# Performance work log

Measured on AMD Instinct MI355X. Metric: run time of the kernel, lower is better.

Reference implementation:

```python
import jax, jax.numpy as jnp
import numpy as np

EMBED = 1024
HEADS = 16
HEAD_DIM = EMBED // HEADS


def setup_inputs() -> dict:
    key = jax.random.key(0)
    ks = jax.random.split(key, 9)
    s = 1.0 / np.sqrt(EMBED)
    inp = {
        "inputs": jax.random.normal(ks[0], (2, 2048, EMBED), dtype=jnp.float32),
        "Wq": jax.random.normal(ks[1], (EMBED, EMBED), dtype=jnp.float32) * s,
        "bq": jnp.zeros((EMBED,), dtype=jnp.float32),
        "Wk": jax.random.normal(ks[2], (EMBED, EMBED), dtype=jnp.float32) * s,
        "bk": jnp.zeros((EMBED,), dtype=jnp.float32),
        "Wv": jax.random.normal(ks[3], (EMBED, EMBED), dtype=jnp.float32) * s,
        "bv": jnp.zeros((EMBED,), dtype=jnp.float32),
        "Wo": jax.random.normal(ks[4], (EMBED, EMBED), dtype=jnp.float32) * s,
        "bo": jnp.zeros((EMBED,), dtype=jnp.float32),
    }
    return inp


def _split_heads(x, B, S):
    # [B, S, E] -> [B, H, S, D]
    return x.reshape(B, S, HEADS, HEAD_DIM).transpose(0, 2, 1, 3)


def reference(inputs, Wq, bq, Wk, bk, Wv, bv, Wo, bo):
    B, S, E = inputs.shape
    q = _split_heads(inputs @ Wq + bq, B, S)
    k = _split_heads(inputs @ Wk + bk, B, S)
    v = _split_heads(inputs @ Wv + bv, B, S)
    # scaled dot-product attention per the original: score scaled by sqrt(d_k)
    score = jnp.einsum("bhsd,bhtd->bhst", q, k) / jnp.sqrt(jnp.float32(HEAD_DIM))
    weights = jax.nn.softmax(score, axis=-1)
    attn = jnp.einsum("bhst,bhtd->bhsd", weights, v)
    concat = attn.transpose(0, 2, 1, 3).reshape(B, S, E)
    return concat @ Wo + bo
```

## Files before the change

### kernel.cpp

```cpp
#include <hip/hip_runtime.h>
#include <cmath>

#define EMBED 1024
#define HEADS 16
#define HDIM  64
#define BATCH 2
#define SEQ   2048
#define MTOT  (BATCH*SEQ)
#define KDIM  1024

typedef __attribute__((ext_vector_type(8))) short bf16x8;
typedef __attribute__((ext_vector_type(4))) float fx4;

#define MFMA(a,b,c) __builtin_amdgcn_mfma_f32_16x16x32_bf16((a),(b),(c),0,0,0)

__device__ __forceinline__ unsigned short f2bf(float x) {
    unsigned u = __float_as_uint(x);
    unsigned r = (u + 0x7FFFu + ((u >> 16) & 1u)) >> 16;
    return (unsigned short)r;
}
__device__ __forceinline__ float bf2f(unsigned short h) {
    return __uint_as_float(((unsigned)h) << 16);
}
__device__ __forceinline__ int swz_grp(int row, int grp) {
    return row * 64 + ((grp ^ (row & 7)) << 3);
}
__device__ __forceinline__ void gload16(const void* g, void* l) {
    __builtin_amdgcn_global_load_lds((const __attribute__((address_space(1))) void*)g,
                                     (__attribute__((address_space(3))) void*)l, 16, 0, 0);
}
__device__ __forceinline__ float dpp_qswap(float x) {
    return __int_as_float(__builtin_amdgcn_mov_dpp(__float_as_int(x), 0xB1, 0xF, 0xF, true));
}

#define C2S 0.18033688f

__global__ __launch_bounds__(256)
void prep(const float* __restrict__ X,
          const float* __restrict__ Wq, const float* __restrict__ Wk,
          const float* __restrict__ Wv, const float* __restrict__ Wo,
          unsigned short* __restrict__ Xh,
          unsigned short* __restrict__ WtH, unsigned short* __restrict__ WtOh)
{
    const int bid = blockIdx.x;
    const int tid = threadIdx.x;
    if (bid < 2048) {
        int i = (bid * 256 + tid) * 8;
        float4 a = *(const float4*)(X + i);
        float4 b = *(const float4*)(X + i + 4);
        bf16x8 h;
        h[0] = (short)f2bf(a.x); h[1] = (short)f2bf(a.y);
        h[2] = (short)f2bf(a.z); h[3] = (short)f2bf(a.w);
        h[4] = (short)f2bf(b.x); h[5] = (short)f2bf(b.y);
        h[6] = (short)f2bf(b.z); h[7] = (short)f2bf(b.w);
        *(bf16x8*)(Xh + i) = h;
        return;
    }
    const int u = bid - 2048;
    const int z = u >> 8;
    const float* W = (z == 0) ? Wq : (z == 1) ? Wk : (z == 2) ? Wv : Wo;
    unsigned short* Th = (z < 3) ? WtH + (size_t)z * 1048576 : WtOh;
    const int k0 = ((u >> 4) & 15) * 64, n0 = (u & 15) * 64;

    __shared__ float t[64][65];
    #pragma unroll
    for (int it = 0; it < 4; ++it) {
        int v2 = tid + it * 256;
        int r = v2 >> 4, c4 = (v2 & 15) << 2;
        float4 v = *(const float4*)(W + (size_t)(k0 + r) * EMBED + n0 + c4);
        t[r][c4] = v.x; t[r][c4 + 1] = v.y; t[r][c4 + 2] = v.z; t[r][c4 + 3] = v.w;
    }
    __syncthreads();
    #pragma unroll
    for (int it = 0; it < 4; ++it) {
        int v2 = tid + it * 256;
        int r = v2 >> 4, c4 = (v2 & 15) << 2;
        ushort4 h;
        h.x = f2bf(t[c4 + 0][r]);
        h.y = f2bf(t[c4 + 1][r]);
        h.z = f2bf(t[c4 + 2][r]);
        h.w = f2bf(t[c4 + 3][r]);
        *(ushort4*)(Th + (size_t)(n0 + r) * EMBED + k0 + c4) = h;
    }
}

__global__ __launch_bounds__(256, 4)
void gemm_qkv(const unsigned short* __restrict__ Xh,
              const unsigned short* __restrict__ WtH,
              const float* __restrict__ bq, const float* __restrict__ bk,
              const float* __restrict__ bv,
              unsigned short* __restrict__ Qh, unsigned short* __restrict__ Khi,
              unsigned short* __restrict__ Vhi)
{
    __shared__ unsigned short Ah[8192];
    __shared__ unsigned short Bh[4096];

    const int tid = threadIdx.x, lane = tid & 63, w = tid >> 6;
    const int wm = w >> 1, wn = w & 1;
    const int which = blockIdx.y;
    const int lin = (blockIdx.x & 7) * 64 + (blockIdx.x >> 3);
    const int m0 = (lin >> 4) * 128, n0 = (lin & 15) * 64;

    const char* aB  = (const char*)(Xh + (size_t)m0 * KDIM);
    const char* bB  = (const char*)(WtH + (size_t)which * 1048576 + (size_t)n0 * KDIM);

    auto stageA = [&](int kt) {
        #pragma unroll
        for (int i = 0; i < 4; ++i) {
            int uw = (i << 12) + (w << 10);
            int u  = uw + (lane << 4);
            int row = u >> 7, grp = (u >> 4) & 7;
            size_t gb = (size_t)row * (KDIM * 2) + (size_t)kt * 128 + ((grp ^ (row & 7)) << 4);
            gload16(aB + gb, (char*)Ah + uw);
        }
    };
    auto stageB = [&](int kt) {
        #pragma unroll
        for (int i = 0; i < 2; ++i) {
            int uw = (i << 12) + (w << 10);
            int u  = uw + (lane << 4);
            int row = u >> 7, grp = (u >> 4) & 7;
            size_t gb = (size_t)row * (KDIM * 2) + (size_t)kt * 128 + ((grp ^ (row & 7)) << 4);
            gload16(bB + gb, (char*)Bh + uw);
        }
    };

    const fx4 zero4 = {0.f, 0.f, 0.f, 0.f};
    fx4 acc[4][2];
    #pragma unroll
    for (int i = 0; i < 4; ++i) { acc[i][0] = zero4; acc[i][1] = zero4; }

    for (int kt = 0; kt < KDIM / 64; ++kt) {
        __syncthreads();
        stageA(kt);
        stageB(kt);
        __syncthreads();
        #pragma unroll
        for (int kh = 0; kh < 2; ++kh) {
            const int grp = kh * 4 + (lane >> 4);
            bf16x8 ah[4], bh2[2];
            #pragma unroll
            for (int mi = 0; mi < 4; ++mi)
                ah[mi] = *(const bf16x8*)(Ah + swz_grp(wm * 64 + mi * 16 + (lane & 15), grp));
            #pragma unroll
            for (int ni = 0; ni < 2; ++ni)
                bh2[ni] = *(const bf16x8*)(Bh + swz_grp(wn * 32 + ni * 16 + (lane & 15), grp));
            #pragma unroll
            for (int mi = 0; mi < 4; ++mi)
                #pragma unroll
                for (int ni = 0; ni < 2; ++ni)
                    acc[mi][ni] = MFMA(ah[mi], bh2[ni], acc[mi][ni]);
        }
    }

    const int hh = n0 >> 6;
    const float* bias = (which == 0) ? bq : (which == 1) ? bk : bv;
    #pragma unroll
    for (int mi = 0; mi < 4; ++mi)
        #pragma unroll
        for (int ni = 0; ni < 2; ++ni) {
            const int n = n0 + wn * 32 + ni * 16 + (lane & 15);
            const float bb = bias[n];
            const int d = n & 63;
            if (which < 2) {
                unsigned short* plane = (which == 0) ? Qh : Khi;
                #pragma unroll
                for (int reg = 0; reg < 4; ++reg) {
                    const int m = m0 + wm * 64 + mi * 16 + (lane >> 4) * 4 + reg;
                    const int b = m >> 11, s = m & (SEQ - 1);
                    float val = acc[mi][ni][reg] + bb;
                    if (which == 0) val *= C2S;
                    plane[((size_t)(b * HEADS + hh) * SEQ + s) * HDIM + d] = f2bf(val);
                }
            } else {
                const int m = m0 + wm * 64 + mi * 16 + (lane >> 4) * 4;
                const int b = m >> 11, s = m & (SEQ - 1);
                const int sl = s & 63;
                const int c = (sl & 32) | ((sl & 12) << 1) | ((sl & 16) >> 2);
                ushort4 o;
                o.x = f2bf(acc[mi][ni][0] + bb);
                o.y = f2bf(acc[mi][ni][1] + bb);
                o.z = f2bf(acc[mi][ni][2] + bb);
                o.w = f2bf(acc[mi][ni][3] + bb);
                *(ushort4*)(Vhi + ((size_t)(b * HEADS + hh) * HDIM + d) * SEQ
                            + (s & ~63) + c) = o;
            }
        }
}

__global__ __launch_bounds__(256, 4)
void gemm_ao(const unsigned short* __restrict__ AOh,
             const unsigned short* __restrict__ Bgh,
             const float* __restrict__ bias, float* __restrict__ Cf)
{
    __shared__ unsigned short Ah[8192];
    __shared__ unsigned short Bh[4096];

    const int tid = threadIdx.x, lane = tid & 63, w = tid >> 6;
    const int wm = w >> 1, wn = w & 1;
    const int lin = (blockIdx.x & 7) * 64 + (blockIdx.x >> 3);
    const int m0 = (lin >> 4) * 128, n0 = (lin & 15) * 64;

    const char* aB = (const char*)(AOh + (size_t)m0 * KDIM);
    const char* bB = (const char*)(Bgh + (size_t)n0 * KDIM);

    auto stageA = [&](int kt) {
        #pragma unroll
        for (int i = 0; i < 4; ++i) {
            int uw = (i << 12) + (w << 10);
            int u  = uw + (lane << 4);
            int row = u >> 7, grp = (u >> 4) & 7;
            size_t gb = (size_t)row * (KDIM * 2) + (size_t)kt * 128 + ((grp ^ (row & 7)) << 4);
            gload16(aB + gb, (char*)Ah + uw);
        }
    };
    auto stageB = [&](int kt) {
        #pragma unroll
        for (int i = 0; i < 2; ++i) {
            int uw = (i << 12) + (w << 10);
            int u  = uw + (lane << 4);
            int row = u >> 7, grp = (u >> 4) & 7;
            size_t gb = (size_t)row * (KDIM * 2) + (size_t)kt * 128 + ((grp ^ (row & 7)) << 4);
            gload16(bB + gb, (char*)Bh + uw);
        }
    };

    const fx4 zero4 = {0.f, 0.f, 0.f, 0.f};
    fx4 acc[4][2];
    #pragma unroll
    for (int i = 0; i < 4; ++i) { acc[i][0] = zero4; acc[i][1] = zero4; }

    for (int kt = 0; kt < KDIM / 64; ++kt) {
        __syncthreads();
        stageA(kt);
        stageB(kt);
        __syncthreads();
        #pragma unroll
        for (int kh = 0; kh < 2; ++kh) {
            const int grp = kh * 4 + (lane >> 4);
            bf16x8 ah[4], bh2[2];
            #pragma unroll
            for (int mi = 0; mi < 4; ++mi)
                ah[mi] = *(const bf16x8*)(Ah + swz_grp(wm * 64 + mi * 16 + (lane & 15), grp));
            #pragma unroll
            for (int ni = 0; ni < 2; ++ni)
                bh2[ni] = *(const bf16x8*)(Bh + swz_grp(wn * 32 + ni * 16 + (lane & 15), grp));
            #pragma unroll
            for (int mi = 0; mi < 4; ++mi)
                #pragma unroll
                for (int ni = 0; ni < 2; ++ni)
                    acc[mi][ni] = MFMA(ah[mi], bh2[ni], acc[mi][ni]);
        }
    }

    #pragma unroll
    for (int mi = 0; mi < 4; ++mi)
        #pragma unroll
        for (int ni = 0; ni < 2; ++ni) {
            const int n = n0 + wn * 32 + ni * 16 + (lane & 15);
            const float bb = bias[n];
            #pragma unroll
            for (int reg = 0; reg < 4; ++reg) {
                const int m = m0 + wm * 64 + mi * 16 + (lane >> 4) * 4 + reg;
                Cf[(size_t)m * EMBED + n] = acc[mi][ni][reg] + bb;
            }
        }
}

__global__ __launch_bounds__(256, 4)
void attn_mfma(const unsigned short* __restrict__ Qh,
               const unsigned short* __restrict__ Khi,
               const unsigned short* __restrict__ Vhi, unsigned short* __restrict__ AOh)
{
    __shared__ unsigned short Ks[2][4096];
    __shared__ unsigned short Vs[2][4096];

    const int tid = threadIdx.x, lane = tid & 63, w = tid >> 6;
    const int xcd = blockIdx.x & 7, loc = blockIdx.x >> 3;
    const int bh = xcd * 4 + (loc >> 5);
    const int q0 = (loc & 31) * 64;
    const size_t qkBase = (size_t)bh * SEQ * HDIM;

    auto stageKV = [&](int kv0, int buf) {
        const char* baseK = (const char*)(Khi + qkBase + (size_t)kv0 * HDIM);
        const char* baseV = (const char*)(Vhi + (size_t)bh * HDIM * SEQ + kv0);
        #pragma unroll
        for (int i = 0; i < 2; ++i) {
            int uw = (i << 12) + (w << 10);
            int u  = uw + (lane << 4);
            int row = u >> 7, grp = (u >> 4) & 7;
            size_t gk = (size_t)row * 128 + ((grp ^ (row & 7)) << 4);
            size_t gv = (size_t)row * (SEQ * 2) + ((grp ^ (row & 7)) << 4);
            gload16(baseK + gk, (char*)Ks[buf] + uw);
            gload16(baseV + gv, (char*)Vs[buf] + uw);
        }
    };

    bf16x8 qf[2];
    #pragma unroll
    for (int kh = 0; kh < 2; ++kh) {
        const int row = q0 + w * 16 + (lane & 15);
        const int grp = kh * 4 + (lane >> 4);
        qf[kh] = *(const bf16x8*)(Qh + qkBase + (size_t)row * HDIM + grp * 8);
    }

    const fx4 zero4 = {0.f, 0.f, 0.f, 0.f};
    fx4 acco[4];
    fx4 accl = zero4;
    #pragma unroll
    for (int df = 0; df < 4; ++df) acco[df] = zero4;

    bf16x8 ones;
    #pragma unroll
    for (int i = 0; i < 8; ++i) ones[i] = (short)0x3F80;

    stageKV(0, 0);
    __syncthreads();

    for (int t = 0; t < 32; ++t) {
        const int cur = t & 1;
        if (t < 31) stageKV((t + 1) * 64, cur ^ 1);

        fx4 s4[4] = {zero4, zero4, zero4, zero4};
        __builtin_amdgcn_s_setprio(1);
        #pragma unroll
        for (int kh = 0; kh < 2; ++kh) {
            const int grp = kh * 4 + (lane >> 4);
            bf16x8 kf[4];
            #pragma unroll
            for (int nf = 0; nf < 4; ++nf)
                kf[nf] = *(const bf16x8*)(Ks[cur] + swz_grp(nf * 16 + (lane & 15), grp));
            #pragma unroll
            for (int nf = 0; nf < 4; ++nf)
                s4[nf] = MFMA(kf[nf], qf[kh], s4[nf]);
        }
        __builtin_amdgcn_s_setprio(0);

        float p[4][4];
        #pragma unroll
        for (int kvf = 0; kvf < 4; ++kvf)
            #pragma unroll
            for (int reg = 0; reg < 4; ++reg) {
                float e;
                asm("v_exp_f32 %0, %1\n\ts_nop 0" : "=v"(e) : "v"(s4[kvf][reg]));
                p[kvf][reg] = e;
            }

        bf16x8 pa[2];
        #pragma unroll
        for (int t2 = 0; t2 < 2; ++t2) {
            union { unsigned u[4]; bf16x8 v; } pk;
            asm("v_cvt_pk_bf16_f32 %0, %1, %2" : "=v"(pk.u[0])
                : "v"(p[2 * t2][0]), "v"(p[2 * t2][1]));
            asm("v_cvt_pk_bf16_f32 %0, %1, %2" : "=v"(pk.u[1])
                : "v"(p[2 * t2][2]), "v"(p[2 * t2][3]));
            asm("v_cvt_pk_bf16_f32 %0, %1, %2" : "=v"(pk.u[2])
                : "v"(p[2 * t2 + 1][0]), "v"(p[2 * t2 + 1][1]));
            asm("v_cvt_pk_bf16_f32 %0, %1, %2" : "=v"(pk.u[3])
                : "v"(p[2 * t2 + 1][2]), "v"(p[2 * t2 + 1][3]));
            pa[t2] = pk.v;
        }

        __builtin_amdgcn_s_setprio(1);
        #pragma unroll
        for (int t2 = 0; t2 < 2; ++t2) {
            const int grp = t2 * 4 + (lane >> 4);
            accl = MFMA(pa[t2], ones, accl);
            #pragma unroll
            for (int df = 0; df < 4; ++df) {
                bf16x8 vh = *(const bf16x8*)(Vs[cur] + swz_grp(df * 16 + (lane & 15), grp));
                acco[df] = MFMA(pa[t2], vh, acco[df]);
            }
        }
        __builtin_amdgcn_s_setprio(0);

        __syncthreads();
    }

    const int b = bh >> 4, h = bh & 15;
    const int parity = lane & 1;
    float inv[4];
    #pragma unroll
    for (int reg = 0; reg < 4; ++reg) inv[reg] = __builtin_amdgcn_rcpf(accl[reg]);
    #pragma unroll
    for (int df = 0; df < 4; ++df) {
        const int d0 = df * 16 + ((lane & 15) & ~1);
        #pragma unroll
        for (int rp = 0; rp < 4; rp += 2) {
            float ve = acco[df][rp]     * inv[rp];
            float vo = acco[df][rp + 1] * inv[rp + 1];
            float e_sw = dpp_qswap(ve), o_sw = dpp_qswap(vo);
            float a  = parity ? o_sw : ve;
            float b2 = parity ? vo   : e_sw;
            unsigned u;
            asm volatile("v_cvt_pk_bf16_f32 %0, %1, %2" : "=v"(u) : "v"(a), "v"(b2));
            const int q = q0 + w * 16 + (lane >> 4) * 4 + rp + parity;
            *(unsigned int*)(AOh + ((size_t)(b * SEQ + q) * EMBED + h * HDIM + d0)) = u;
        }
    }
}

extern "C" void kernel_launch(void* const* d_in, const int* in_sizes, int n_in,
                              void* d_out, int out_size, void* d_ws, size_t ws_size,
                              hipStream_t stream)
{
    (void)in_sizes; (void)n_in; (void)out_size; (void)ws_size;

    const float* X  = (const float*)d_in[0];
    const float* Wq = (const float*)d_in[1];
    const float* bq = (const float*)d_in[2];
    const float* Wk = (const float*)d_in[3];
    const float* bk = (const float*)d_in[4];
    const float* Wv = (const float*)d_in[5];
    const float* bv = (const float*)d_in[6];
    const float* Wo = (const float*)d_in[7];
    const float* bo = (const float*)d_in[8];

    const size_t R_us = (size_t)8 * 1024 * 1024;
    unsigned short* us = (unsigned short*)d_ws;
    unsigned short* Qh   = us + 0 * R_us;
    unsigned short* WtOh = us + 0 * R_us + 4194304;
    unsigned short* Khi  = us + 1 * R_us;
    unsigned short* Vhi  = us + 2 * R_us;
    unsigned short* AOh  = us + 3 * R_us;
    unsigned short* WtH  = us + 3 * R_us;
    unsigned short* Xh   = (unsigned short*)d_out;

    const dim3 blk(256);

    prep<<<dim3(3072), blk, 0, stream>>>(X, Wq, Wk, Wv, Wo, Xh, WtH, WtOh);

    gemm_qkv<<<dim3(512, 3), blk, 0, stream>>>(Xh, WtH, bq, bk, bv, Qh, Khi, Vhi);

    attn_mfma<<<dim3(1024), blk, 0, stream>>>(Qh, Khi, Vhi, AOh);

    gemm_ao<<<dim3(512), blk, 0, stream>>>(AOh, WtOh, bo, (float*)d_out);
}
```

Measured before the change: 110.3 us.

## Enlarge QKV GEMM tile to 128x128 and use 8-wave attention blocks

The QKV projection GEMM moves from 128x64 to 128x128 output tiles, so each wave computes a 64x64 sub-tile with 16 accumulators and each A tile loaded from shared memory feeds more MFMAs. Launch bounds drop to 3 blocks per SM to fit the extra registers and LDS. The attention kernel moves to 512-thread blocks covering 128 query rows, so each staged K/V tile is shared by twice as many query rows and each thread issues one load per stage instead of two. The costs are lower occupancy and fewer blocks in flight for the GEMM, and larger blocks for attention.

```diff
diff --git a/kernel.cpp b/kernel.cpp
--- a/kernel.cpp
+++ b/kernel.cpp
@@ -84,7 +84,7 @@
     }
 }
 
-__global__ __launch_bounds__(256, 4)
+__global__ __launch_bounds__(256, 3)
 void gemm_qkv(const unsigned short* __restrict__ Xh,
               const unsigned short* __restrict__ WtH,
               const float* __restrict__ bq, const float* __restrict__ bk,
@@ -93,16 +93,16 @@
               unsigned short* __restrict__ Vhi)
 {
     __shared__ unsigned short Ah[8192];
-    __shared__ unsigned short Bh[4096];
+    __shared__ unsigned short Bh[8192];
 
     const int tid = threadIdx.x, lane = tid & 63, w = tid >> 6;
     const int wm = w >> 1, wn = w & 1;
     const int which = blockIdx.y;
-    const int lin = (blockIdx.x & 7) * 64 + (blockIdx.x >> 3);
-    const int m0 = (lin >> 4) * 128, n0 = (lin & 15) * 64;
-
-    const char* aB  = (const char*)(Xh + (size_t)m0 * KDIM);
-    const char* bB  = (const char*)(WtH + (size_t)which * 1048576 + (size_t)n0 * KDIM);
+    const int lin = (blockIdx.x & 7) * 32 + (blockIdx.x >> 3);
+    const int m0 = (lin >> 3) * 128, n0 = (lin & 7) * 128;
+
+    const char* aB = (const char*)(Xh + (size_t)m0 * KDIM);
+    const char* bB = (const char*)(WtH + (size_t)which * 1048576 + (size_t)n0 * KDIM);
 
     auto stageA = [&](int kt) {
         #pragma unroll
@@ -116,7 +116,7 @@
     };
     auto stageB = [&](int kt) {
         #pragma unroll
-        for (int i = 0; i < 2; ++i) {
+        for (int i = 0; i < 4; ++i) {
             int uw = (i << 12) + (w << 10);
             int u  = uw + (lane << 4);
             int row = u >> 7, grp = (u >> 4) & 7;
@@ -126,9 +126,11 @@
     };
 
     const fx4 zero4 = {0.f, 0.f, 0.f, 0.f};
-    fx4 acc[4][2];
-    #pragma unroll
-    for (int i = 0; i < 4; ++i) { acc[i][0] = zero4; acc[i][1] = zero4; }
+    fx4 acc[4][4];
+    #pragma unroll
+    for (int i = 0; i < 4; ++i)
+        #pragma unroll
+        for (int j = 0; j < 4; ++j) acc[i][j] = zero4;
 
     for (int kt = 0; kt < KDIM / 64; ++kt) {
         __syncthreads();
@@ -138,30 +140,29 @@
         #pragma unroll
         for (int kh = 0; kh < 2; ++kh) {
             const int grp = kh * 4 + (lane >> 4);
-            bf16x8 ah[4], bh2[2];
+            bf16x8 ah[4], bh4[4];
             #pragma unroll
             for (int mi = 0; mi < 4; ++mi)
                 ah[mi] = *(const bf16x8*)(Ah + swz_grp(wm * 64 + mi * 16 + (lane & 15), grp));
             #pragma unroll
-            for (int ni = 0; ni < 2; ++ni)
-                bh2[ni] = *(const bf16x8*)(Bh + swz_grp(wn * 32 + ni * 16 + (lane & 15), grp));
+            for (int ni = 0; ni < 4; ++ni)
+                bh4[ni] = *(const bf16x8*)(Bh + swz_grp(wn * 64 + ni * 16 + (lane & 15), grp));
             #pragma unroll
             for (int mi = 0; mi < 4; ++mi)
                 #pragma unroll
-                for (int ni = 0; ni < 2; ++ni)
-                    acc[mi][ni] = MFMA(ah[mi], bh2[ni], acc[mi][ni]);
-        }
-    }
-
-    const int hh = n0 >> 6;
+                for (int ni = 0; ni < 4; ++ni)
+                    acc[mi][ni] = MFMA(ah[mi], bh4[ni], acc[mi][ni]);
+        }
+    }
+
     const float* bias = (which == 0) ? bq : (which == 1) ? bk : bv;
     #pragma unroll
     for (int mi = 0; mi < 4; ++mi)
         #pragma unroll
-        for (int ni = 0; ni < 2; ++ni) {
-            const int n = n0 + wn * 32 + ni * 16 + (lane & 15);
+        for (int ni = 0; ni < 4; ++ni) {
+            const int n = n0 + wn * 64 + ni * 16 + (lane & 15);
             const float bb = bias[n];
-            const int d = n & 63;
+            const int hh = n >> 6, d = n & 63;
             if (which < 2) {
                 unsigned short* plane = (which == 0) ? Qh : Khi;
                 #pragma unroll
@@ -267,7 +268,7 @@
         }
 }
 
-__global__ __launch_bounds__(256, 4)
+__global__ __launch_bounds__(512, 8)
 void attn_mfma(const unsigned short* __restrict__ Qh,
                const unsigned short* __restrict__ Khi,
                const unsigned short* __restrict__ Vhi, unsigned short* __restrict__ AOh)
@@ -277,23 +278,20 @@
 
     const int tid = threadIdx.x, lane = tid & 63, w = tid >> 6;
     const int xcd = blockIdx.x & 7, loc = blockIdx.x >> 3;
-    const int bh = xcd * 4 + (loc >> 5);
-    const int q0 = (loc & 31) * 64;
+    const int bh = xcd * 4 + (loc >> 4);
+    const int q0 = (loc & 15) * 128;
     const size_t qkBase = (size_t)bh * SEQ * HDIM;
 
     auto stageKV = [&](int kv0, int buf) {
         const char* baseK = (const char*)(Khi + qkBase + (size_t)kv0 * HDIM);
         const char* baseV = (const char*)(Vhi + (size_t)bh * HDIM * SEQ + kv0);
-        #pragma unroll
-        for (int i = 0; i < 2; ++i) {
-            int uw = (i << 12) + (w << 10);
-            int u  = uw + (lane << 4);
-            int row = u >> 7, grp = (u >> 4) & 7;
-            size_t gk = (size_t)row * 128 + ((grp ^ (row & 7)) << 4);
-            size_t gv = (size_t)row * (SEQ * 2) + ((grp ^ (row & 7)) << 4);
-            gload16(baseK + gk, (char*)Ks[buf] + uw);
-            gload16(baseV + gv, (char*)Vs[buf] + uw);
-        }
+        const int uw = w << 10;
+        const int u  = uw + (lane << 4);
+        const int row = u >> 7, grp = (u >> 4) & 7;
+        const size_t gk = (size_t)row * 128 + ((grp ^ (row & 7)) << 4);
+        const size_t gv = (size_t)row * (SEQ * 2) + ((grp ^ (row & 7)) << 4);
+        gload16(baseK + gk, (char*)Ks[buf] + uw);
+        gload16(baseV + gv, (char*)Vs[buf] + uw);
     };
 
     bf16x8 qf[2];
@@ -426,13 +424,11 @@
     unsigned short* WtH  = us + 3 * R_us;
     unsigned short* Xh   = (unsigned short*)d_out;
 
-    const dim3 blk(256);
-
-    prep<<<dim3(3072), blk, 0, stream>>>(X, Wq, Wk, Wv, Wo, Xh, WtH, WtOh);
-
-    gemm_qkv<<<dim3(512, 3), blk, 0, stream>>>(Xh, WtH, bq, bk, bv, Qh, Khi, Vhi);
-
-    attn_mfma<<<dim3(1024), blk, 0, stream>>>(Qh, Khi, Vhi, AOh);
-
-    gemm_ao<<<dim3(512), blk, 0, stream>>>(AOh, WtOh, bo, (float*)d_out);
-}
+    prep<<<dim3(3072), dim3(256), 0, stream>>>(X, Wq, Wk, Wv, Wo, Xh, WtH, WtOh);
+
+    gemm_qkv<<<dim3(256, 3), dim3(256), 0, stream>>>(Xh, WtH, bq, bk, bv, Qh, Khi, Vhi);
+
+    attn_mfma<<<dim3(512), dim3(512), 0, stream>>>(Qh, Khi, Vhi, AOh);
+
+    gemm_ao<<<dim3(512), dim3(256), 0, stream>>>(AOh, WtOh, bo, (float*)d_out);
+}
```

After: 101.8 us. -7.7%, faster.
